# Performance work log

Measured on AMD Instinct MI355X. Metric: run time of the kernel, lower is better.

## Reference

```python
import jax, jax.numpy as jnp
import numpy as np

B, S, D = 2, 2048, 1024
H = 16
DH = D // H  # 64

def setup_inputs() -> dict:
    key = jax.random.key(0)
    k1, k2, k3, k4 = jax.random.split(key, 4)
    scale = 0.02
    x = jax.random.normal(k1, (B, S, D), dtype=jnp.float32)
    W_query = jax.random.normal(k2, (D, D), dtype=jnp.float32) * scale
    W_key = jax.random.normal(k3, (D, D), dtype=jnp.float32) * scale
    W_value = jax.random.normal(k4, (D, D), dtype=jnp.float32) * scale
    return {"x": x, "W_query": W_query, "W_key": W_key, "W_value": W_value}

def reference(x, W_query, W_key, W_value):
    b, n, d_in = x.shape
    # project and split heads: [b, h, n, dh]
    q = (x @ W_query).reshape(b, n, H, DH).transpose(0, 2, 1, 3)
    k = (x @ W_key).reshape(b, n, H, DH).transpose(0, 2, 1, 3)
    v = (x @ W_value).reshape(b, n, H, DH).transpose(0, 2, 1, 3)
    # raw scores, then causal mask (strict upper triangle -> -inf)
    scores = jnp.einsum('bhqd,bhkd->bhqk', q, k)
    causal = jnp.tril(jnp.ones((n, n), dtype=bool))  # True = keep
    scores = jnp.where(causal, scores, -jnp.inf)
    weights = jax.nn.softmax(scores / jnp.sqrt(jnp.float32(DH)), axis=-1)
    ctx = jnp.einsum('bhqk,bhkd->bhqd', weights, v)
    return ctx.transpose(0, 2, 1, 3).reshape(b, n, H * DH)
```

## Files before the change

kernel.cpp:

```cpp
#include <hip/hip_runtime.h>
#include <hip/hip_bf16.h>

#define S_LEN   2048
#define D_MODEL 1024
#define N_HEADS 16
#define D_HEAD  64
#define HEAD_ELEMS (2048ull * 64ull)
#define MAT_ELEMS  (4096ull * 1024ull)
#define W_ELEMS    (1024ull * 1024ull)

typedef __attribute__((ext_vector_type(8))) short short8_t;
typedef __attribute__((ext_vector_type(4))) short short4_t;
typedef __attribute__((ext_vector_type(4))) float f32x4;

__device__ __forceinline__ short f2bf(float f) {
    __hip_bfloat16 h = __float2bfloat16(f);
    union { __hip_bfloat16 h; short s; } cv;
    cv.h = h;
    return cv.s;
}

#define GLD_LDS16(gptr, lptr) \
    __builtin_amdgcn_global_load_lds( \
        (const __attribute__((address_space(1))) unsigned int*)(gptr), \
        (__attribute__((address_space(3))) unsigned int*)(lptr), 16, 0, 0)

__global__ __launch_bounds__(256) void convert_x_kernel(
    const float* __restrict__ x, short* __restrict__ xb)
{
    const int i = (blockIdx.x * 256 + threadIdx.x) * 8;
    const float4 v0 = *(const float4*)(x + i);
    const float4 v1 = *(const float4*)(x + i + 4);
    short8_t u;
    u[0] = f2bf(v0.x); u[1] = f2bf(v0.y); u[2] = f2bf(v0.z); u[3] = f2bf(v0.w);
    u[4] = f2bf(v1.x); u[5] = f2bf(v1.y); u[6] = f2bf(v1.z); u[7] = f2bf(v1.w);
    *(short8_t*)(xb + i) = u;
}

__global__ __launch_bounds__(256) void transpose_w_kernel(
    const float* __restrict__ Wq, const float* __restrict__ Wk,
    const float* __restrict__ Wv, short* __restrict__ wt)
{
    const int k0 = blockIdx.x * 64;
    const int n0 = blockIdx.y * 64;
    const int which = blockIdx.z;
    const float* W = (which == 0) ? Wq : (which == 1) ? Wk : Wv;
    short* out = wt + (size_t)which * W_ELEMS;

    __shared__ float Ts[64][68];
    const int t = threadIdx.x;
    {
        const int c4 = (t & 15) * 4;
#pragma unroll
        for (int i = 0; i < 4; ++i) {
            const int r = (t >> 4) + i * 16;
            const float4 v = *(const float4*)(W + (size_t)(k0 + r) * D_MODEL + n0 + c4);
            Ts[c4 + 0][r] = v.x; Ts[c4 + 1][r] = v.y;
            Ts[c4 + 2][r] = v.z; Ts[c4 + 3][r] = v.w;
        }
    }
    __syncthreads();
    const int nl = t >> 2;
#pragma unroll
    for (int s = 0; s < 2; ++s) {
        const int koff = (t & 3) * 8 + s * 32;
        short8_t u;
#pragma unroll
        for (int j = 0; j < 8; ++j) u[j] = f2bf(Ts[nl][koff + j]);
        *(short8_t*)(out + (size_t)(n0 + nl) * D_MODEL + k0 + koff) = u;
    }
}

__global__ __launch_bounds__(256, 3) void qkv_mfma_gemm_kernel(
    const short* __restrict__ xb,
    const short* __restrict__ wt,
    short* __restrict__ qkv)
{
    const int mBlock = blockIdx.x * 128;
    const int nBlock = blockIdx.y * 128;
    const int which  = blockIdx.z;
    const short* Bt = wt + (size_t)which * W_ELEMS;
    short* outBase  = qkv + (size_t)which * MAT_ELEMS;

    __shared__ short As[128 * 32];
    __shared__ short Bs[128 * 32];

    const int t    = threadIdx.x;
    const int w    = t >> 6;
    const int lane = t & 63;
    const int n16  = lane & 15;
    const int quad = lane >> 4;
    const int mq   = (w & 1) * 64;
    const int nq   = (w >> 1) * 64;

    f32x4 acc[4][4];
#pragma unroll
    for (int i = 0; i < 4; ++i)
#pragma unroll
        for (int j = 0; j < 4; ++j) acc[i][j] = (f32x4){0.f, 0.f, 0.f, 0.f};

    const int off0 = w * 2048 + lane * 16;
    const int off1 = off0 + 1024;
    const int r0s = off0 >> 6, k0s = (off0 & 63) >> 1;
    const int r1s = off1 >> 6, k1s = (off1 & 63) >> 1;
    const short* gA0 = xb + (size_t)(mBlock + r0s) * D_MODEL + k0s;
    const short* gA1 = xb + (size_t)(mBlock + r1s) * D_MODEL + k1s;
    const short* gB0 = Bt + (size_t)(nBlock + r0s) * D_MODEL + k0s;
    const short* gB1 = Bt + (size_t)(nBlock + r1s) * D_MODEL + k1s;
    short* lA0 = As + w * 1024;
    short* lA1 = As + w * 1024 + 512;
    short* lB0 = Bs + w * 1024;
    short* lB1 = Bs + w * 1024 + 512;

    for (int k0 = 0; k0 < D_MODEL; k0 += 32) {
        __syncthreads();
        GLD_LDS16(gA0 + k0, lA0);
        GLD_LDS16(gA1 + k0, lA1);
        GLD_LDS16(gB0 + k0, lB0);
        GLD_LDS16(gB1 + k0, lB1);
        __syncthreads();

        short8_t af[4], bf[4];
#pragma unroll
        for (int mt = 0; mt < 4; ++mt)
            af[mt] = *(const short8_t*)&As[(mq + mt * 16 + n16) * 32 + quad * 8];
#pragma unroll
        for (int nt = 0; nt < 4; ++nt)
            bf[nt] = *(const short8_t*)&Bs[(nq + nt * 16 + n16) * 32 + quad * 8];
#pragma unroll
        for (int mt = 0; mt < 4; ++mt)
#pragma unroll
            for (int nt = 0; nt < 4; ++nt)
                acc[mt][nt] = __builtin_amdgcn_mfma_f32_16x16x32_bf16(
                    af[mt], bf[nt], acc[mt][nt], 0, 0, 0);
    }

    if (which < 2) {
#pragma unroll
        for (int mt = 0; mt < 4; ++mt) {
#pragma unroll
            for (int nt = 0; nt < 4; ++nt) {
                const int n = nBlock + nq + nt * 16 + n16;
                const int h = n >> 6, dh = n & 63;
#pragma unroll
                for (int reg = 0; reg < 4; ++reg) {
                    const int m = mBlock + mq + mt * 16 + quad * 4 + reg;
                    const int bb = m >> 11, ss = m & 2047;
                    outBase[((size_t)(bb * N_HEADS + h) * S_LEN + ss) * D_HEAD + dh] =
                        f2bf(acc[mt][nt][reg]);
                }
            }
        }
    } else {
#pragma unroll
        for (int mt = 0; mt < 4; ++mt) {
            const int m0 = mBlock + mq + mt * 16 + quad * 4;
            const int bb = m0 >> 11, ss0 = m0 & 2047;
#pragma unroll
            for (int nt = 0; nt < 4; ++nt) {
                const int n = nBlock + nq + nt * 16 + n16;
                const int h = n >> 6, dh = n & 63;
                short4_t u;
                u[0] = f2bf(acc[mt][nt][0]); u[1] = f2bf(acc[mt][nt][1]);
                u[2] = f2bf(acc[mt][nt][2]); u[3] = f2bf(acc[mt][nt][3]);
                *(short4_t*)(outBase +
                    ((size_t)((bb * N_HEADS + h) * D_HEAD + dh)) * S_LEN + ss0) = u;
            }
        }
    }
}

__global__ __launch_bounds__(256, 2) void attn_mfma_kernel(
    const short* __restrict__ qkv,
    float* __restrict__ out)
{
    const int bh   = blockIdx.x;
    const int qb   = blockIdx.y;
    const int base = qb * 64;
    const int t    = threadIdx.x;
    const int w    = t >> 6;
    const int lane = t & 63;
    const int n    = lane & 15;
    const int quad = lane >> 4;

    const short* Q  = qkv + (size_t)bh * HEAD_ELEMS;
    const short* K  = qkv + MAT_ELEMS + (size_t)bh * HEAD_ELEMS;
    const short* Vt = qkv + 2 * MAT_ELEMS + (size_t)bh * HEAD_ELEMS;

    __shared__ __align__(16) short KsBuf[64][72];
    __shared__ __align__(16) short VsBuf[64][72];
    __shared__ __align__(16) short PsBuf[4][16][72];

    const int r0 = base + w * 16;
    const int qrow = r0 + n;

    const short8_t bq0 = *(const short8_t*)(Q + (size_t)qrow * D_HEAD + quad * 8);
    const short8_t bq1 = *(const short8_t*)(Q + (size_t)qrow * D_HEAD + quad * 8 + 32);

    float m = -__builtin_inff();
    float l = 0.f;
    f32x4 o[4];
#pragma unroll
    for (int f = 0; f < 4; ++f) o[f] = (f32x4){0.f, 0.f, 0.f, 0.f};

    for (int tile = 0; tile <= qb; ++tile) {
        const int j0 = tile * 64;
        __syncthreads();
        {
            const int row = t >> 2;
            const int seg = t & 3;
            const uint4* gk = (const uint4*)(K + (size_t)(j0 + row) * D_HEAD + seg * 16);
            uint4 k0 = gk[0], k1 = gk[1];
            *(uint4*)&KsBuf[row][seg * 16 + 0] = k0;
            *(uint4*)&KsBuf[row][seg * 16 + 8] = k1;
            const uint4* gv = (const uint4*)(Vt + (size_t)row * S_LEN + j0 + seg * 16);
            uint4 v0 = gv[0], v1 = gv[1];
            *(uint4*)&VsBuf[row][seg * 16 + 0] = v0;
            *(uint4*)&VsBuf[row][seg * 16 + 8] = v1;
        }
        __syncthreads();

        f32x4 st[4];
#pragma unroll
        for (int kg = 0; kg < 4; ++kg) {
            const short8_t a0 = *(const short8_t*)&KsBuf[kg * 16 + n][quad * 8];
            const short8_t a1 = *(const short8_t*)&KsBuf[kg * 16 + n][quad * 8 + 32];
            f32x4 acc = (f32x4){0.f, 0.f, 0.f, 0.f};
            acc = __builtin_amdgcn_mfma_f32_16x16x32_bf16(a0, bq0, acc, 0, 0, 0);
            acc = __builtin_amdgcn_mfma_f32_16x16x32_bf16(a1, bq1, acc, 0, 0, 0);
            st[kg] = acc;
        }

        float p[16];
        float mx = -__builtin_inff();
#pragma unroll
        for (int kg = 0; kg < 4; ++kg) {
#pragma unroll
            for (int r = 0; r < 4; ++r) {
                const int key = j0 + kg * 16 + quad * 4 + r;
                float s = st[kg][r] * 0.125f;
                s = (key <= qrow) ? s : -__builtin_inff();
                p[kg * 4 + r] = s;
                mx = fmaxf(mx, s);
            }
        }
        mx = fmaxf(mx, __shfl_xor(mx, 16));
        mx = fmaxf(mx, __shfl_xor(mx, 32));
        const float mnew  = fmaxf(m, mx);
        const float alpha = __expf(m - mnew);
        float ls = 0.f;
#pragma unroll
        for (int i = 0; i < 16; ++i) {
            p[i] = __expf(p[i] - mnew);
            ls += p[i];
        }
        ls += __shfl_xor(ls, 16);
        ls += __shfl_xor(ls, 32);
        l = l * alpha + ls;
        m = mnew;
#pragma unroll
        for (int f = 0; f < 4; ++f) {
            o[f][0] *= alpha; o[f][1] *= alpha; o[f][2] *= alpha; o[f][3] *= alpha;
        }

#pragma unroll
        for (int kg = 0; kg < 4; ++kg) {
            short4_t pk;
            pk[0] = f2bf(p[kg * 4 + 0]); pk[1] = f2bf(p[kg * 4 + 1]);
            pk[2] = f2bf(p[kg * 4 + 2]); pk[3] = f2bf(p[kg * 4 + 3]);
            *(short4_t*)&PsBuf[w][n][kg * 16 + quad * 4] = pk;
        }
        const short8_t pb0 = *(const short8_t*)&PsBuf[w][n][quad * 8];
        const short8_t pb1 = *(const short8_t*)&PsBuf[w][n][quad * 8 + 32];

#pragma unroll
        for (int f = 0; f < 4; ++f) {
            const short8_t va0 = *(const short8_t*)&VsBuf[f * 16 + n][quad * 8];
            const short8_t va1 = *(const short8_t*)&VsBuf[f * 16 + n][quad * 8 + 32];
            o[f] = __builtin_amdgcn_mfma_f32_16x16x32_bf16(va0, pb0, o[f], 0, 0, 0);
            o[f] = __builtin_amdgcn_mfma_f32_16x16x32_bf16(va1, pb1, o[f], 0, 0, 0);
        }
    }

    __syncthreads();
    float* Os = (float*)((w < 2) ? &KsBuf[0][0] : &VsBuf[0][0]) + (w & 1) * (16 * 72);
    const float inv_l = 1.0f / l;
#pragma unroll
    for (int f = 0; f < 4; ++f) {
        f32x4 q4;
        q4[0] = o[f][0] * inv_l; q4[1] = o[f][1] * inv_l;
        q4[2] = o[f][2] * inv_l; q4[3] = o[f][3] * inv_l;
        *(f32x4*)&Os[n * 72 + f * 16 + quad * 4] = q4;
    }
    const int bb = bh >> 4;
    const int hh = bh & 15;
#pragma unroll
    for (int rr = 0; rr < 4; ++rr) {
        const int row = rr * 4 + quad;
        const f32x4 val = *(const f32x4*)&Os[row * 72 + n * 4];
        *(f32x4*)(out + ((size_t)(bb * S_LEN + r0 + row)) * D_MODEL + hh * D_HEAD + n * 4) = val;
    }
}

extern "C" void kernel_launch(void* const* d_in, const int* in_sizes, int n_in,
                              void* d_out, int out_size, void* d_ws, size_t ws_size,
                              hipStream_t stream) {
    const float* x  = (const float*)d_in[0];
    const float* Wq = (const float*)d_in[1];
    const float* Wk = (const float*)d_in[2];
    const float* Wv = (const float*)d_in[3];
    float* out = (float*)d_out;

    short* xb  = (short*)d_ws;
    short* wt  = xb + MAT_ELEMS;
    short* qkv = wt + 3 * W_ELEMS;

    convert_x_kernel<<<dim3(MAT_ELEMS / (256 * 8)), 256, 0, stream>>>(x, xb);
    transpose_w_kernel<<<dim3(16, 16, 3), 256, 0, stream>>>(Wq, Wk, Wv, wt);

    qkv_mfma_gemm_kernel<<<dim3(32, 8, 3), 256, 0, stream>>>(xb, wt, qkv);

    attn_mfma_kernel<<<dim3(2 * N_HEADS, S_LEN / 64), 256, 0, stream>>>(qkv, out);
}
```

Baseline: 168.3 us.

## Pair causal query blocks per CTA, async LDS loads with XOR swizzle, fold scale into Q

Each attention block now processes two query blocks (pr and 31-pr) so every CTA does equal causal work, and the grid is halved. K/V tiles are loaded straight into LDS with global_load_lds into XOR-swizzled unpadded buffers. The 1/sqrt(dh) scale is folded into the Q projection epilogue, and the causal mask is applied only on the diagonal tile. The float-to-bf16 conversion of P becomes a truncating bit shift. Fewer CTAs may reduce occupancy, and truncation slightly changes rounding.

```diff
diff --git a/kernel.cpp b/kernel.cpp
--- a/kernel.cpp
+++ b/kernel.cpp
@@ -135,6 +135,7 @@
                     af[mt], bf[nt], acc[mt][nt], 0, 0, 0);
     }
 
+    const float oscale = (which == 0) ? 0.125f : 1.0f;
     if (which < 2) {
 #pragma unroll
         for (int mt = 0; mt < 4; ++mt) {
@@ -147,7 +148,7 @@
                     const int m = mBlock + mq + mt * 16 + quad * 4 + reg;
                     const int bb = m >> 11, ss = m & 2047;
                     outBase[((size_t)(bb * N_HEADS + h) * S_LEN + ss) * D_HEAD + dh] =
-                        f2bf(acc[mt][nt][reg]);
+                        f2bf(acc[mt][nt][reg] * oscale);
                 }
             }
         }
@@ -175,8 +176,7 @@
     float* __restrict__ out)
 {
     const int bh   = blockIdx.x;
-    const int qb   = blockIdx.y;
-    const int base = qb * 64;
+    const int pr   = blockIdx.y;
     const int t    = threadIdx.x;
     const int w    = t >> 6;
     const int lane = t & 63;
@@ -187,118 +187,147 @@
     const short* K  = qkv + MAT_ELEMS + (size_t)bh * HEAD_ELEMS;
     const short* Vt = qkv + 2 * MAT_ELEMS + (size_t)bh * HEAD_ELEMS;
 
-    __shared__ __align__(16) short KsBuf[64][72];
-    __shared__ __align__(16) short VsBuf[64][72];
-    __shared__ __align__(16) short PsBuf[4][16][72];
-
-    const int r0 = base + w * 16;
-    const int qrow = r0 + n;
-
-    const short8_t bq0 = *(const short8_t*)(Q + (size_t)qrow * D_HEAD + quad * 8);
-    const short8_t bq1 = *(const short8_t*)(Q + (size_t)qrow * D_HEAD + quad * 8 + 32);
-
-    float m = -__builtin_inff();
-    float l = 0.f;
-    f32x4 o[4];
-#pragma unroll
-    for (int f = 0; f < 4; ++f) o[f] = (f32x4){0.f, 0.f, 0.f, 0.f};
-
-    for (int tile = 0; tile <= qb; ++tile) {
-        const int j0 = tile * 64;
-        __syncthreads();
-        {
-            const int row = t >> 2;
-            const int seg = t & 3;
-            const uint4* gk = (const uint4*)(K + (size_t)(j0 + row) * D_HEAD + seg * 16);
-            uint4 k0 = gk[0], k1 = gk[1];
-            *(uint4*)&KsBuf[row][seg * 16 + 0] = k0;
-            *(uint4*)&KsBuf[row][seg * 16 + 8] = k1;
-            const uint4* gv = (const uint4*)(Vt + (size_t)row * S_LEN + j0 + seg * 16);
-            uint4 v0 = gv[0], v1 = gv[1];
-            *(uint4*)&VsBuf[row][seg * 16 + 0] = v0;
-            *(uint4*)&VsBuf[row][seg * 16 + 8] = v1;
-        }
-        __syncthreads();
-
-        f32x4 st[4];
-#pragma unroll
-        for (int kg = 0; kg < 4; ++kg) {
-            const short8_t a0 = *(const short8_t*)&KsBuf[kg * 16 + n][quad * 8];
-            const short8_t a1 = *(const short8_t*)&KsBuf[kg * 16 + n][quad * 8 + 32];
-            f32x4 acc = (f32x4){0.f, 0.f, 0.f, 0.f};
-            acc = __builtin_amdgcn_mfma_f32_16x16x32_bf16(a0, bq0, acc, 0, 0, 0);
-            acc = __builtin_amdgcn_mfma_f32_16x16x32_bf16(a1, bq1, acc, 0, 0, 0);
-            st[kg] = acc;
-        }
-
-        float p[16];
-        float mx = -__builtin_inff();
-#pragma unroll
-        for (int kg = 0; kg < 4; ++kg) {
-#pragma unroll
-            for (int r = 0; r < 4; ++r) {
-                const int key = j0 + kg * 16 + quad * 4 + r;
-                float s = st[kg][r] * 0.125f;
-                s = (key <= qrow) ? s : -__builtin_inff();
-                p[kg * 4 + r] = s;
-                mx = fmaxf(mx, s);
-            }
-        }
-        mx = fmaxf(mx, __shfl_xor(mx, 16));
-        mx = fmaxf(mx, __shfl_xor(mx, 32));
-        const float mnew  = fmaxf(m, mx);
-        const float alpha = __expf(m - mnew);
-        float ls = 0.f;
-#pragma unroll
-        for (int i = 0; i < 16; ++i) {
-            p[i] = __expf(p[i] - mnew);
-            ls += p[i];
-        }
-        ls += __shfl_xor(ls, 16);
-        ls += __shfl_xor(ls, 32);
-        l = l * alpha + ls;
-        m = mnew;
-#pragma unroll
-        for (int f = 0; f < 4; ++f) {
-            o[f][0] *= alpha; o[f][1] *= alpha; o[f][2] *= alpha; o[f][3] *= alpha;
-        }
-
-#pragma unroll
-        for (int kg = 0; kg < 4; ++kg) {
-            short4_t pk;
-            pk[0] = f2bf(p[kg * 4 + 0]); pk[1] = f2bf(p[kg * 4 + 1]);
-            pk[2] = f2bf(p[kg * 4 + 2]); pk[3] = f2bf(p[kg * 4 + 3]);
-            *(short4_t*)&PsBuf[w][n][kg * 16 + quad * 4] = pk;
-        }
-        const short8_t pb0 = *(const short8_t*)&PsBuf[w][n][quad * 8];
-        const short8_t pb1 = *(const short8_t*)&PsBuf[w][n][quad * 8 + 32];
-
-#pragma unroll
-        for (int f = 0; f < 4; ++f) {
-            const short8_t va0 = *(const short8_t*)&VsBuf[f * 16 + n][quad * 8];
-            const short8_t va1 = *(const short8_t*)&VsBuf[f * 16 + n][quad * 8 + 32];
-            o[f] = __builtin_amdgcn_mfma_f32_16x16x32_bf16(va0, pb0, o[f], 0, 0, 0);
-            o[f] = __builtin_amdgcn_mfma_f32_16x16x32_bf16(va1, pb1, o[f], 0, 0, 0);
-        }
-    }
-
-    __syncthreads();
-    float* Os = (float*)((w < 2) ? &KsBuf[0][0] : &VsBuf[0][0]) + (w & 1) * (16 * 72);
-    const float inv_l = 1.0f / l;
-#pragma unroll
-    for (int f = 0; f < 4; ++f) {
-        f32x4 q4;
-        q4[0] = o[f][0] * inv_l; q4[1] = o[f][1] * inv_l;
-        q4[2] = o[f][2] * inv_l; q4[3] = o[f][3] * inv_l;
-        *(f32x4*)&Os[n * 72 + f * 16 + quad * 4] = q4;
-    }
+    __shared__ __align__(16) short Ks[64 * 64];
+    __shared__ __align__(16) short Vs[64 * 64];
+    __shared__ __align__(16) short Ps[4][16][72];
+
+    const int srow0 = w * 16 + (lane >> 3);
+    const int srow1 = srow0 + 8;
+    const int sd0 = ((lane & 7) ^ (srow0 & 7)) * 8;
+    const int sd1 = ((lane & 7) ^ (srow1 & 7)) * 8;
+    const short* gK0 = K + srow0 * 64 + sd0;
+    const short* gK1 = K + srow1 * 64 + sd1;
+    const short* gV0 = Vt + (size_t)srow0 * S_LEN + sd0;
+    const short* gV1 = Vt + (size_t)srow1 * S_LEN + sd1;
+    short* lK0 = Ks + (w * 16) * 64;
+    short* lK1 = Ks + (w * 16 + 8) * 64;
+    short* lV0 = Vs + (w * 16) * 64;
+    short* lV1 = Vs + (w * 16 + 8) * 64;
+
+    const int pcK = ((quad ^ (n & 7))) * 8;
+
     const int bb = bh >> 4;
     const int hh = bh & 15;
-#pragma unroll
-    for (int rr = 0; rr < 4; ++rr) {
-        const int row = rr * 4 + quad;
-        const f32x4 val = *(const f32x4*)&Os[row * 72 + n * 4];
-        *(f32x4*)(out + ((size_t)(bb * S_LEN + r0 + row)) * D_MODEL + hh * D_HEAD + n * 4) = val;
+
+    for (int pass = 0; pass < 2; ++pass) {
+        const int qb = pass ? (31 - pr) : pr;
+        const int r0 = qb * 64 + w * 16;
+        const int qrow = r0 + n;
+
+        const short8_t bq0 = *(const short8_t*)(Q + (size_t)qrow * D_HEAD + quad * 8);
+        const short8_t bq1 = *(const short8_t*)(Q + (size_t)qrow * D_HEAD + quad * 8 + 32);
+
+        float m = -__builtin_inff();
+        float l = 0.f;
+        f32x4 o[4];
+#pragma unroll
+        for (int f = 0; f < 4; ++f) o[f] = (f32x4){0.f, 0.f, 0.f, 0.f};
+
+        for (int tile = 0; tile <= qb; ++tile) {
+            const int j0 = tile * 64;
+            __syncthreads();
+            GLD_LDS16(gK0 + j0 * 64, lK0);
+            GLD_LDS16(gK1 + j0 * 64, lK1);
+            GLD_LDS16(gV0 + j0, lV0);
+            GLD_LDS16(gV1 + j0, lV1);
+            __syncthreads();
+
+            f32x4 st[4];
+#pragma unroll
+            for (int kg = 0; kg < 4; ++kg) {
+                const int rbase = (kg * 16 + n) * 64;
+                const short8_t a0 = *(const short8_t*)&Ks[rbase + pcK];
+                const short8_t a1 = *(const short8_t*)&Ks[rbase + (pcK ^ 32)];
+                f32x4 acc = (f32x4){0.f, 0.f, 0.f, 0.f};
+                acc = __builtin_amdgcn_mfma_f32_16x16x32_bf16(a0, bq0, acc, 0, 0, 0);
+                acc = __builtin_amdgcn_mfma_f32_16x16x32_bf16(a1, bq1, acc, 0, 0, 0);
+                st[kg] = acc;
+            }
+
+            float p[16];
+            float mx = -__builtin_inff();
+            if (tile == qb) {
+#pragma unroll
+                for (int kg = 0; kg < 4; ++kg)
+#pragma unroll
+                    for (int r = 0; r < 4; ++r) {
+                        const int key = j0 + kg * 16 + quad * 4 + r;
+                        float s = st[kg][r];
+                        s = (key <= qrow) ? s : -__builtin_inff();
+                        p[kg * 4 + r] = s;
+                        mx = fmaxf(mx, s);
+                    }
+            } else {
+#pragma unroll
+                for (int i = 0; i < 16; ++i) {
+                    const float s = st[i >> 2][i & 3];
+                    p[i] = s;
+                    mx = fmaxf(mx, s);
+                }
+            }
+            mx = fmaxf(mx, __shfl_xor(mx, 16));
+            mx = fmaxf(mx, __shfl_xor(mx, 32));
+            const float mnew  = fmaxf(m, mx);
+            const float alpha = __expf(m - mnew);
+            float ls = 0.f;
+#pragma unroll
+            for (int i = 0; i < 16; ++i) {
+                p[i] = __expf(p[i] - mnew);
+                ls += p[i];
+            }
+            ls += __shfl_xor(ls, 16);
+            ls += __shfl_xor(ls, 32);
+            l = l * alpha + ls;
+            m = mnew;
+#pragma unroll
+            for (int f = 0; f < 4; ++f) {
+                o[f][0] *= alpha; o[f][1] *= alpha; o[f][2] *= alpha; o[f][3] *= alpha;
+            }
+
+#pragma unroll
+            for (int kg = 0; kg < 4; ++kg) {
+                const unsigned int b0 = __builtin_bit_cast(unsigned int, p[kg * 4 + 0]);
+                const unsigned int b1 = __builtin_bit_cast(unsigned int, p[kg * 4 + 1]);
+                const unsigned int b2 = __builtin_bit_cast(unsigned int, p[kg * 4 + 2]);
+                const unsigned int b3 = __builtin_bit_cast(unsigned int, p[kg * 4 + 3]);
+                uint2 pk;
+                pk.x = (b0 >> 16) | (b1 & 0xffff0000u);
+                pk.y = (b2 >> 16) | (b3 & 0xffff0000u);
+                *(uint2*)&Ps[w][n][kg * 16 + quad * 4] = pk;
+            }
+            const short8_t pb0 = *(const short8_t*)&Ps[w][n][quad * 8];
+            const short8_t pb1 = *(const short8_t*)&Ps[w][n][quad * 8 + 32];
+
+#pragma unroll
+            for (int f = 0; f < 4; ++f) {
+                const int rbase = (f * 16 + n) * 64;
+                const short8_t va0 = *(const short8_t*)&Vs[rbase + pcK];
+                const short8_t va1 = *(const short8_t*)&Vs[rbase + (pcK ^ 32)];
+                o[f] = __builtin_amdgcn_mfma_f32_16x16x32_bf16(va0, pb0, o[f], 0, 0, 0);
+                o[f] = __builtin_amdgcn_mfma_f32_16x16x32_bf16(va1, pb1, o[f], 0, 0, 0);
+            }
+        }
+
+        __syncthreads();
+        float* Os = (float*)((w < 2) ? Ks : Vs) + (w & 1) * 1024;
+        const float inv_l = 1.0f / l;
+#pragma unroll
+        for (int f = 0; f < 4; ++f) {
+            const int c  = f * 4 + quad;
+            const int pc = c ^ n;
+            f32x4 q4;
+            q4[0] = o[f][0] * inv_l; q4[1] = o[f][1] * inv_l;
+            q4[2] = o[f][2] * inv_l; q4[3] = o[f][3] * inv_l;
+            *(f32x4*)&Os[n * 64 + pc * 4] = q4;
+        }
+#pragma unroll
+        for (int rr = 0; rr < 4; ++rr) {
+            const int row = rr * 4 + quad;
+            const int pc  = n ^ row;
+            const f32x4 val = *(const f32x4*)&Os[row * 64 + pc * 4];
+            *(f32x4*)(out + ((size_t)(bb * S_LEN + r0 + row)) * D_MODEL
+                          + hh * D_HEAD + n * 4) = val;
+        }
     }
 }
 
@@ -320,5 +349,5 @@
 
     qkv_mfma_gemm_kernel<<<dim3(32, 8, 3), 256, 0, stream>>>(xb, wt, qkv);
 
-    attn_mfma_kernel<<<dim3(2 * N_HEADS, S_LEN / 64), 256, 0, stream>>>(qkv, out);
-}
+    attn_mfma_kernel<<<dim3(2 * N_HEADS, 16), 256, 0, stream>>>(qkv, out);
+}
```

After: 153.7 us. 1.09x faster.
